# Kernel optimization log

Hardware: AMD Instinct MI355X
Metric: run time of the kernel (lower is better)

## Reference

```python
import jax, jax.numpy as jnp
import numpy as np

B, S, D_X, D_H = 1024, 512, 128, 128
A_VOCAB, A_EMB, T_VOCAB, T_EMB = 100, 32, 4, 16
GRU_IN = D_X + A_EMB + T_EMB + 1  # 177
Y_IN = D_H + D_X + A_EMB + T_EMB  # 304


def _lin_init(key, d_in, d_out):
    k1, k2 = jax.random.split(key)
    lim = 1.0 / np.sqrt(d_in)
    W = jax.random.uniform(k1, (d_out, d_in), minval=-lim, maxval=lim, dtype=jnp.float32)
    b = jax.random.uniform(k2, (d_out,), minval=-lim, maxval=lim, dtype=jnp.float32)
    return W, b


def setup_inputs() -> dict:
    key = jax.random.key(0)
    ks = jax.random.split(key, 16)
    x = jax.random.normal(ks[0], (B, D_X), dtype=jnp.float32)
    a = jax.random.randint(ks[1], (B, S), 0, A_VOCAB)
    t = jax.random.randint(ks[2], (B, S), 0, T_VOCAB)
    y = jax.random.uniform(ks[3], (B, S), dtype=jnp.float32)
    mask = jnp.ones((B, S), dtype=jnp.float32)

    xW, xb = _lin_init(ks[4], D_X, D_X)                 # x_proj
    a_emb = jax.random.normal(ks[5], (A_VOCAB, A_EMB), dtype=jnp.float32)
    t_emb = jax.random.normal(ks[6], (T_VOCAB, T_EMB), dtype=jnp.float32)
    W_ih, b_ih = _lin_init(ks[7], GRU_IN, 3 * D_H)      # GRUCell input weights
    W_hh, b_hh = _lin_init(ks[8], D_H, 3 * D_H)         # GRUCell hidden weights
    h0W, h0b = _lin_init(ks[9], D_X, D_H)               # h0 MLP
    tW1, tb1 = _lin_init(ks[10], D_H, D_H)              # t_head
    tW2, tb2 = _lin_init(ks[11], D_H, T_VOCAB)
    yW1, yb1 = _lin_init(ks[12], Y_IN, D_H)             # y_head
    yW2, yb2 = _lin_init(ks[13], D_H, 1)
    return {
        'x': x, 'a': a, 't': t, 'y': y, 'mask': mask,
        'xW': xW, 'xb': xb, 'a_emb': a_emb, 't_emb': t_emb,
        'W_ih': W_ih, 'b_ih': b_ih, 'W_hh': W_hh, 'b_hh': b_hh,
        'h0W': h0W, 'h0b': h0b,
        'tW1': tW1, 'tb1': tb1, 'tW2': tW2, 'tb2': tb2,
        'yW1': yW1, 'yb1': yb1, 'yW2': yW2, 'yb2': yb2,
    }


def _crn_forward(x, y, mask, xW, xb, a_emb, t_emb, W_ih, b_ih, W_hh, b_hh,
                 h0W, h0b, tW1, tb1, tW2, tb2, yW1, yb1, yW2, yb2, a, t):
    gelu = lambda v: jax.nn.gelu(v, approximate=False)
    x_enc = x @ xW.T + xb                       # [B, D_X]
    h = jnp.tanh(x_enc @ h0W.T + h0b)           # [B, D_H]
    a_e = a_emb[a]                              # [B, S, A_EMB]
    t_e = t_emb[t]                              # [B, S, T_EMB]
    y3 = y[..., None]                           # [B, S, 1]

    # time-major slices for scan
    a_e_t = jnp.swapaxes(a_e, 0, 1)
    t_e_t = jnp.swapaxes(t_e, 0, 1)
    y_t = jnp.swapaxes(y3, 0, 1)
    m_t = jnp.swapaxes(mask, 0, 1)[..., None]   # [S, B, 1]

    def step(h, inp):
        ae, te, yt, m = inp
        # grad_reverse is identity in forward; dropout off (eval)
        t_logits = gelu(h @ tW1.T + tb1) @ tW2.T + tb2          # [B, T_VOCAB]
        y_in = jnp.concatenate([h, x_enc, ae, te], axis=-1)
        y_logits = gelu(y_in @ yW1.T + yb1) @ yW2.T + yb2        # [B, 1]
        upd = jnp.concatenate([x_enc, ae, te, yt], axis=-1)      # [B, GRU_IN]
        gx = upd @ W_ih.T + b_ih
        gh = h @ W_hh.T + b_hh
        r = jax.nn.sigmoid(gx[:, :D_H] + gh[:, :D_H])
        z = jax.nn.sigmoid(gx[:, D_H:2 * D_H] + gh[:, D_H:2 * D_H])
        n = jnp.tanh(gx[:, 2 * D_H:] + r * gh[:, 2 * D_H:])
        h_next = (1.0 - z) * n + z * h
        h_new = m * h_next + (1.0 - m) * h
        return h_new, (y_logits, t_logits, h)

    _, (y_seq, t_seq, h_seq) = jax.lax.scan(step, h, (a_e_t, t_e_t, y_t, m_t))
    # back to batch-major [B, S, ...]
    return (jnp.swapaxes(y_seq, 0, 1), jnp.swapaxes(t_seq, 0, 1), jnp.swapaxes(h_seq, 0, 1))


def reference(x, a, t, y, mask, xW, xb, a_emb, t_emb, W_ih, b_ih, W_hh, b_hh,
              h0W, h0b, tW1, tb1, tW2, tb2, yW1, yb1, yW2, yb2):
    return _crn_forward(x, y, mask, xW, xb, a_emb, t_emb, W_ih, b_ih, W_hh, b_hh,
                        h0W, h0b, tW1, tb1, tW2, tb2, yW1, yb1, yW2, yb2, a, t)
```

## Files before the change

### kernel.cpp

```cpp
#include <hip/hip_runtime.h>
#include <math.h>

#define SLEN 512

typedef _Float16 half8 __attribute__((ext_vector_type(8)));
typedef _Float16 half2v __attribute__((ext_vector_type(2)));
typedef __fp16 fp16x2 __attribute__((ext_vector_type(2)));
typedef float f32x4 __attribute__((ext_vector_type(4)));
typedef unsigned int uint;

union U4H8 { uint4 u; half8 h; };
union UH2 { uint u; half2v v; fp16x2 p; };

static __device__ __forceinline__ uint packh2(float a, float b){
  UH2 x; x.p = __builtin_amdgcn_cvt_pkrtz(a, b); return x.u;
}
static __device__ __forceinline__ float loh(uint u){ UH2 x; x.u=u; return (float)x.v[0]; }
static __device__ __forceinline__ float hih(uint u){ UH2 x; x.u=u; return (float)x.v[1]; }
static __device__ __forceinline__ half8 ld_h8(const uint* p){
  U4H8 x; x.u = *(const uint4*)p; return x.h;
}
static __device__ __forceinline__ float rcpf(float x){ return __builtin_amdgcn_rcpf(x); }
static __device__ __forceinline__ float sigm(float v){ return rcpf(1.0f+__expf(-v)); }
static __device__ __forceinline__ float tanh_f(float v){ return 1.0f - 2.0f*rcpf(__expf(2.0f*v)+1.0f); }
static __device__ __forceinline__ float gelu_exact(float v){
  return 0.5f*v*(1.0f+erff(v*0.7071067811865475f));
}
#define MFMA(a,b,c) __builtin_amdgcn_mfma_f32_16x16x32_f16((a),(b),(c),0,0,0)

static __device__ __forceinline__ void wg_sync(){
  asm volatile("s_waitcnt lgkmcnt(0)" ::: "memory");
  __builtin_amdgcn_s_barrier();
}

__global__ void k_sample(const float* __restrict__ x, const float* __restrict__ xW, const float* __restrict__ xb,
                         const float* __restrict__ h0W, const float* __restrict__ h0b,
                         const float* __restrict__ W_ih, const float* __restrict__ b_ih, const float* __restrict__ b_hh,
                         const float* __restrict__ yW1, const float* __restrict__ yb1,
                         float* __restrict__ w_h0, float* __restrict__ w_xgx, float* __restrict__ w_yx)
{
  const int b = blockIdx.x, tid = threadIdx.x;
  __shared__ float sx[128];
  __shared__ float sxe[128];
  if (tid < 128) sx[tid] = x[b*128+tid];
  __syncthreads();
  if (tid < 128) {
    float acc = xb[tid];
    #pragma unroll 8
    for (int j=0;j<128;++j) acc += xW[tid*128+j]*sx[j];
    sxe[tid] = acc;
  }
  __syncthreads();
  {
    const int o = tid;
    float acc = b_ih[o] + (o < 256 ? b_hh[o] : 0.f);
    #pragma unroll 8
    for (int j=0;j<128;++j) acc += W_ih[o*177+j]*sxe[j];
    w_xgx[b*384+o] = acc;
  }
  if (tid < 128) {
    float acc = h0b[tid];
    #pragma unroll 8
    for (int j=0;j<128;++j) acc += h0W[tid*128+j]*sxe[j];
    w_h0[b*128+tid] = tanhf(acc);
    float a2 = yb1[tid];
    #pragma unroll 8
    for (int j=0;j<128;++j) a2 += yW1[tid*304+128+j]*sxe[j];
    w_yx[b*128+tid] = a2;
  }
}

__global__ __launch_bounds__(512,1) void k_recur(
  const float* __restrict__ W_hh, const float* __restrict__ W_ih, const float* __restrict__ b_hh,
  const int* __restrict__ a, const int* __restrict__ tt,
  const float* __restrict__ yy, const float* __restrict__ mask,
  const float* __restrict__ w_h0, const float* __restrict__ w_xgx,
  const float* __restrict__ a_emb, const float* __restrict__ t_emb,
  float* __restrict__ o_h, uint* __restrict__ h16)
{
  const int tid = threadIdx.x;
  const int wv = tid>>6, lane = tid&63, q = lane>>4, c = lane&15;
  const int b0 = blockIdx.x*16;
  const int r0 = wv*16;

  __shared__ __align__(16) uint s_h[2][16*68];
  __shared__ __align__(16) uint s_chunk[2][1024];
  __shared__ __align__(16) uint s_al[1600];
  __shared__ __align__(16) uint s_te[32];

  half8 wf[18];
  #pragma unroll
  for (int g=0; g<3; ++g) {
    const int row = g*128 + r0 + c;
    #pragma unroll
    for (int kt=0; kt<4; ++kt) {
      const float4* wp = (const float4*)(W_hh + row*128 + kt*32 + q*8);
      float4 v0 = wp[0], v1 = wp[1];
      half8 hv;
      hv[0]=(_Float16)v0.x; hv[1]=(_Float16)v0.y; hv[2]=(_Float16)v0.z; hv[3]=(_Float16)v0.w;
      hv[4]=(_Float16)v1.x; hv[5]=(_Float16)v1.y; hv[6]=(_Float16)v1.z; hv[7]=(_Float16)v1.w;
      wf[g*6+kt] = hv;
    }
    #pragma unroll
    for (int kt=4; kt<6; ++kt) {
      half8 hv;
      #pragma unroll
      for (int j=0;j<8;++j) {
        int k2 = (kt-4)*32 + q*8 + j;
        float v = (k2 < 49) ? W_ih[row*177 + 128 + k2] : 0.f;
        hv[j] = (_Float16)v;
      }
      wf[g*6+kt] = hv;
    }
  }
  f32x4 xgr, xgz, xgn, bhh, hm;
  #pragma unroll
  for (int j=0;j<4;++j) {
    const int rr = r0 + q*4 + j;
    xgr[j] = w_xgx[(b0+c)*384 +       rr];
    xgz[j] = w_xgx[(b0+c)*384 + 128 + rr];
    xgn[j] = w_xgx[(b0+c)*384 + 256 + rr];
    bhh[j] = b_hh[256 + rr];
    hm[j]  = w_h0[(b0+c)*128 + rr];
  }
  for (int d = tid; d < 1600; d += 512) {
    int row = d>>4, col = d&15;
    s_al[d] = packh2(a_emb[row*32+2*col], a_emb[row*32+2*col+1]);
  }
  if (tid < 32) {
    int row = tid>>3, col = tid&7;
    s_te[tid] = packh2(t_emb[row*16+2*col], t_emb[row*16+2*col+1]);
  }
  uint4 cr0, cr1, cr2, cr3;
  if (wv==0) {
    const uint* bp = (q==0) ? (const uint*)a : (q==1) ? (const uint*)tt
                   : (q==2) ? (const uint*)yy : (const uint*)mask;
    const uint4* p = (const uint4*)(bp + (size_t)(b0+c)*512);
    cr0=p[0]; cr1=p[1]; cr2=p[2]; cr3=p[3];
    uint4* dst = (uint4*)&s_chunk[0][q*256 + c*16];
    dst[0]=cr0; dst[1]=cr1; dst[2]=cr2; dst[3]=cr3;
  }
  s_h[0][c*68 + wv*8 + q*2]     = packh2(hm[0], hm[1]);
  s_h[0][c*68 + wv*8 + q*2 + 1] = packh2(hm[2], hm[3]);
  __syncthreads();

  for (int s=0; s<SLEN; ++s) {
    const int pb = s&1, par = (s>>4)&1, st = s&15;
    half8 hb[4];
    #pragma unroll
    for (int kt=0;kt<4;++kt) hb[kt] = ld_h8(&s_h[pb][c*68 + kt*16 + q*4]);
    const int av = (int)s_chunk[par][c*16 + st];
    const int tv = (int)s_chunk[par][256 + c*16 + st];
    const float yv = __uint_as_float(s_chunk[par][512 + c*16 + st]);
    const float mval = __uint_as_float(s_chunk[par][768 + c*16 + st]);
    half8 eb0 = ld_h8(&s_al[av*16 + q*4]);
    half8 eb1;
    if (q < 2) eb1 = ld_h8(&s_te[tv*8 + q*4]);
    else { U4H8 t; t.u = make_uint4((q==2)?packh2(yv,0.f):0u,0u,0u,0u); eb1 = t.h; }
    {
      const size_t p = (size_t)(b0+c)*SLEN + s;
      if (h16) {
        uint2 u; u.x = packh2(hm[0], hm[1]); u.y = packh2(hm[2], hm[3]);
        *(uint2*)(h16 + p*64 + wv*8 + q*2) = u;
      } else {
        *(float4*)(o_h + p*128 + r0 + q*4) = make_float4(hm[0],hm[1],hm[2],hm[3]);
      }
    }
    f32x4 ar = xgr, az = xgz, anh = bhh, anx = xgn;
    #pragma unroll
    for (int kt=0;kt<4;++kt) {
      ar  = MFMA(wf[kt],      hb[kt], ar);
      az  = MFMA(wf[6+kt],    hb[kt], az);
      anh = MFMA(wf[12+kt],   hb[kt], anh);
    }
    ar  = MFMA(wf[4],  eb0, ar);   ar  = MFMA(wf[5],  eb1, ar);
    az  = MFMA(wf[10], eb0, az);   az  = MFMA(wf[11], eb1, az);
    anx = MFMA(wf[16], eb0, anx);  anx = MFMA(wf[17], eb1, anx);
    #pragma unroll
    for (int j=0;j<4;++j) {
      float rj = sigm(ar[j]), zj = sigm(az[j]);
      float nj = tanh_f(anx[j] + rj*anh[j]);
      float hn = nj + zj*(hm[j] - nj);
      hm[j] = hm[j] + mval*(hn - hm[j]);
    }
    const int nb = (s+1)&1;
    s_h[nb][c*68 + wv*8 + q*2]     = packh2(hm[0], hm[1]);
    s_h[nb][c*68 + wv*8 + q*2 + 1] = packh2(hm[2], hm[3]);
    if (wv==0) {
      if ((st)==8 && s<490) {
        const int s0n = ((s>>4)+1)*16;
        const uint* bp = (q==0) ? (const uint*)a : (q==1) ? (const uint*)tt
                       : (q==2) ? (const uint*)yy : (const uint*)mask;
        const uint4* p = (const uint4*)(bp + (size_t)(b0+c)*512 + s0n);
        cr0=p[0]; cr1=p[1]; cr2=p[2]; cr3=p[3];
      }
      if ((st)==9 && s<491) {
        uint4* dst = (uint4*)&s_chunk[((s>>4)+1)&1][q*256 + c*16];
        dst[0]=cr0; dst[1]=cr1; dst[2]=cr2; dst[3]=cr3;
      }
    }
    wg_sync();
  }
}

template<bool H16>
__global__ __launch_bounds__(256,2) void k_heads(
  const float* __restrict__ tW1, const float* __restrict__ tb1,
  const float* __restrict__ tW2, const float* __restrict__ tb2,
  const float* __restrict__ yW1, const float* __restrict__ yW2, const float* __restrict__ yb2,
  const int* __restrict__ a, const int* __restrict__ tt,
  const float* __restrict__ w_yx,
  const float* __restrict__ a_emb, const float* __restrict__ t_emb,
  const float* __restrict__ h_f32, const uint* __restrict__ h16,
  float* __restrict__ o_y, float* __restrict__ o_t, float* __restrict__ o_h)
{
  const int tid = threadIdx.x;
  const int wv = tid>>6, lane = tid&63, q = lane>>4, c = lane&15;
  const bool isY = (wv >= 2);
  const int uh = wv&1;
  const int pair = wv>>1;
  const int p0 = blockIdx.x*1024;
  const int b0 = blockIdx.x*2;

  __shared__ __align__(16) uint s_al[100*20];
  __shared__ __align__(16) uint s_te[32];
  __shared__ __align__(16) uint s_gb[2][2][16*68];

  for (int d = tid; d < 1600; d += 256) {
    int row = d>>4, col = d&15;
    s_al[row*20+col] = packh2(a_emb[row*32+2*col], a_emb[row*32+2*col+1]);
  }
  if (tid < 32) {
    int row = tid>>3, col = tid&7;
    s_te[row*8+col] = packh2(t_emb[row*16+2*col], t_emb[row*16+2*col+1]);
  }

  half8 wf[24];
  const float* W1 = isY ? yW1 : tW1;
  const int w1stride = isY ? 304 : 128;
  #pragma unroll
  for (int ut=0;ut<4;++ut) {
    const int unit = uh*64 + ut*16 + c;
    #pragma unroll
    for (int kt=0;kt<4;++kt) {
      const float4* wp = (const float4*)(W1 + unit*w1stride + kt*32 + q*8);
      float4 v0 = wp[0], v1 = wp[1];
      half8 hv;
      hv[0]=(_Float16)v0.x; hv[1]=(_Float16)v0.y; hv[2]=(_Float16)v0.z; hv[3]=(_Float16)v0.w;
      hv[4]=(_Float16)v1.x; hv[5]=(_Float16)v1.y; hv[6]=(_Float16)v1.z; hv[7]=(_Float16)v1.w;
      wf[ut*6+kt] = hv;
    }
    #pragma unroll
    for (int kt=4;kt<6;++kt) {
      half8 hv;
      #pragma unroll
      for (int j=0;j<8;++j) {
        int k2 = (kt-4)*32 + q*8 + j;
        float v = (isY && k2 < 48) ? yW1[unit*304 + 256 + k2] : 0.f;
        hv[j] = (_Float16)v;
      }
      wf[ut*6+kt] = hv;
    }
  }
  half8 w2f[4];
  #pragma unroll
  for (int kt=0;kt<4;++kt) {
    half8 hv;
    #pragma unroll
    for (int j=0;j<8;++j) {
      float v = 0.f;
      if (!isY && c < 4) v = tW2[c*128 + kt*32 + q*8 + j];
      if ( isY && c == 0) v = yW2[kt*32 + q*8 + j];
      hv[j] = (_Float16)v;
    }
    w2f[kt] = hv;
  }
  float tb2r[4]; float yb2s = yb2[0];
  #pragma unroll
  for (int r=0;r<4;++r) tb2r[r] = tb2[r];
  f32x4 bsr0[4], bsr1[4];
  #pragma unroll
  for (int ut=0;ut<4;++ut)
    #pragma unroll
    for (int r=0;r<4;++r) {
      const int u = uh*64 + ut*16 + q*4 + r;
      bsr0[ut][r] = isY ? w_yx[(b0+0)*128 + u] : tb1[u];
      bsr1[ut][r] = isY ? w_yx[(b0+1)*128 + u] : tb1[u];
    }

  __syncthreads();

  half8 hbn[4];
  int avn = 0, tvn = 0;
  if (H16) {
    const uint* hp = h16 + (size_t)(p0 + c)*64;
    #pragma unroll
    for (int kt=0;kt<4;++kt) hbn[kt] = ld_h8(hp + kt*16 + q*4);
  }
  if (isY) { avn = a[p0 + c]; tvn = tt[p0 + c]; }

  #pragma unroll 1
  for (int ti=0; ti<64; ++ti) {
    const int par = ti&1;
    const int p = p0 + ti*16 + c;

    half8 hb[4];
    if (H16) {
      #pragma unroll
      for (int kt=0;kt<4;++kt) hb[kt] = hbn[kt];
    } else {
      const float* hp = h_f32 + (size_t)p*128;
      #pragma unroll
      for (int kt=0;kt<4;++kt) {
        const float4* fp = (const float4*)(hp + kt*32 + q*8);
        float4 v0 = fp[0], v1 = fp[1];
        half8 hv;
        hv[0]=(_Float16)v0.x; hv[1]=(_Float16)v0.y; hv[2]=(_Float16)v0.z; hv[3]=(_Float16)v0.w;
        hv[4]=(_Float16)v1.x; hv[5]=(_Float16)v1.y; hv[6]=(_Float16)v1.z; hv[7]=(_Float16)v1.w;
        hb[kt] = hv;
      }
    }
    const int av = avn, tv = tvn;

    if (H16 && !isY) {
      float* op = o_h + (size_t)p*128;
      #pragma unroll
      for (int kk=0;kk<2;++kk) {
        const int kt = uh*2 + kk;
        float4 f0 = make_float4((float)hb[kt][0], (float)hb[kt][1], (float)hb[kt][2], (float)hb[kt][3]);
        float4 f1 = make_float4((float)hb[kt][4], (float)hb[kt][5], (float)hb[kt][6], (float)hb[kt][7]);
        *(float4*)(op + kt*32 + q*8)     = f0;
        *(float4*)(op + kt*32 + q*8 + 4) = f1;
      }
    }

    f32x4 acc[4];
    #pragma unroll
    for (int ut=0;ut<4;++ut) acc[ut] = (ti < 32) ? bsr0[ut] : bsr1[ut];
    #pragma unroll
    for (int kt=0;kt<4;++kt)
      #pragma unroll
      for (int ut=0;ut<4;++ut) acc[ut] = MFMA(wf[ut*6+kt], hb[kt], acc[ut]);
    if (isY) {
      half8 eb[2];
      eb[0] = ld_h8(&s_al[av*20 + q*4]);
      if (q < 2) eb[1] = ld_h8(&s_te[tv*8 + q*4]);
      else {
        half8 z;
        #pragma unroll
        for (int j=0;j<8;++j) z[j] = (_Float16)0.f;
        eb[1] = z;
      }
      #pragma unroll
      for (int kt=4;kt<6;++kt)
        #pragma unroll
        for (int ut=0;ut<4;++ut) acc[ut] = MFMA(wf[ut*6+kt], eb[kt-4], acc[ut]);
    }

    #pragma unroll
    for (int ut=0;ut<4;++ut)
      #pragma unroll
      for (int pr=0;pr<2;++pr) {
        float g0 = gelu_exact(acc[ut][2*pr]);
        float g1 = gelu_exact(acc[ut][2*pr+1]);
        s_gb[pair][par][c*68 + uh*32 + ut*8 + 2*q + pr] = packh2(g0, g1);
      }

    {
      const int tn = (ti < 63) ? ti+1 : 63;
      const int pn = p0 + tn*16 + c;
      if (H16) {
        const uint* hp = h16 + (size_t)pn*64;
        #pragma unroll
        for (int kt=0;kt<4;++kt) hbn[kt] = ld_h8(hp + kt*16 + q*4);
      }
      if (isY) { avn = a[pn]; tvn = tt[pn]; }
    }

    wg_sync();

    if (par == uh) {
      f32x4 a2; a2[0]=0.f; a2[1]=0.f; a2[2]=0.f; a2[3]=0.f;
      #pragma unroll
      for (int kt=0;kt<4;++kt) {
        half8 gb = ld_h8(&s_gb[pair][par][c*68 + kt*16 + q*4]);
        a2 = MFMA(w2f[kt], gb, a2);
      }
      if (lane < 16) {
        if (!isY) {
          float4 o = make_float4(a2[0]+tb2r[0], a2[1]+tb2r[1], a2[2]+tb2r[2], a2[3]+tb2r[3]);
          *(float4*)&o_t[(size_t)p*4] = o;
        } else {
          o_y[p] = a2[0] + yb2s;
        }
      }
    }
  }
}

extern "C" void kernel_launch(void* const* d_in, const int* in_sizes, int n_in,
                              void* d_out, int out_size, void* d_ws, size_t ws_size,
                              hipStream_t stream) {
  (void)in_sizes; (void)n_in; (void)out_size;
  const float* x     = (const float*)d_in[0];
  const int*   a     = (const int*)  d_in[1];
  const int*   tt    = (const int*)  d_in[2];
  const float* y     = (const float*)d_in[3];
  const float* mask  = (const float*)d_in[4];
  const float* xW    = (const float*)d_in[5];
  const float* xb    = (const float*)d_in[6];
  const float* a_emb = (const float*)d_in[7];
  const float* t_emb = (const float*)d_in[8];
  const float* W_ih  = (const float*)d_in[9];
  const float* b_ih  = (const float*)d_in[10];
  const float* W_hh  = (const float*)d_in[11];
  const float* b_hh  = (const float*)d_in[12];
  const float* h0W   = (const float*)d_in[13];
  const float* h0b   = (const float*)d_in[14];
  const float* tW1   = (const float*)d_in[15];
  const float* tb1   = (const float*)d_in[16];
  const float* tW2   = (const float*)d_in[17];
  const float* tb2   = (const float*)d_in[18];
  const float* yW1   = (const float*)d_in[19];
  const float* yb1   = (const float*)d_in[20];
  const float* yW2   = (const float*)d_in[21];
  const float* yb2   = (const float*)d_in[22];

  float* o_y = (float*)d_out;
  float* o_t = o_y + 524288;
  float* o_h = o_y + 2621440;

  float* ws    = (float*)d_ws;
  float* w_h0  = ws;
  float* w_xgx = ws + 131072;
  float* w_yx  = ws + 524288;

  const size_t H16_BYTES = (size_t)524288 * 256;
  uint* h16 = nullptr;
  if (ws_size >= (size_t)655360*4 + H16_BYTES) h16 = (uint*)(ws + 655360);

  k_sample<<<1024, 384, 0, stream>>>(x, xW, xb, h0W, h0b, W_ih, b_ih, b_hh, yW1, yb1,
                                     w_h0, w_xgx, w_yx);
  k_recur<<<64, 512, 0, stream>>>(W_hh, W_ih, b_hh, a, tt, y, mask,
                                  w_h0, w_xgx, a_emb, t_emb, o_h, h16);
  if (h16)
    k_heads<true><<<512, 256, 0, stream>>>(tW1, tb1, tW2, tb2, yW1, yW2, yb2, a, tt,
                                           w_yx, a_emb, t_emb, o_h, h16, o_y, o_t, o_h);
  else
    k_heads<false><<<512, 256, 0, stream>>>(tW1, tb1, tW2, tb2, yW1, yW2, yb2, a, tt,
                                            w_yx, a_emb, t_emb, o_h, nullptr, o_y, o_t, o_h);
}
```

Before: 1.194 ms.

## Fuse output heads into recurrent kernel and swizzle shared-memory layouts

Moves the t-head and y-head computation into the recurrent kernel. Each wave computes its 16-unit slice of the first-layer head projections with extra MFMAs per step, writes GELU outputs to shared memory, and two waves apply the second-layer projection one step later. This removes the separate heads kernel and the fp16 hidden-state round trip through global memory. In exchange, every step of the serial recurrence now carries extra MFMA, GELU and store work, and only 64 workgroups run on a large GPU. Shared-memory layouts also get XOR swizzles and transposed chunk storage to reduce bank conflicts.

```diff
diff --git a/kernel.cpp b/kernel.cpp
--- a/kernel.cpp
+++ b/kernel.cpp
@@ -15,8 +15,6 @@
 static __device__ __forceinline__ uint packh2(float a, float b){
   UH2 x; x.p = __builtin_amdgcn_cvt_pkrtz(a, b); return x.u;
 }
-static __device__ __forceinline__ float loh(uint u){ UH2 x; x.u=u; return (float)x.v[0]; }
-static __device__ __forceinline__ float hih(uint u){ UH2 x; x.u=u; return (float)x.v[1]; }
 static __device__ __forceinline__ half8 ld_h8(const uint* p){
   U4H8 x; x.u = *(const uint4*)p; return x.h;
 }
@@ -26,12 +24,15 @@
 static __device__ __forceinline__ float gelu_exact(float v){
   return 0.5f*v*(1.0f+erff(v*0.7071067811865475f));
 }
+static __device__ __forceinline__ half8 cvt8(const float* p){
+  const float4* fp = (const float4*)p;
+  float4 v0 = fp[0], v1 = fp[1];
+  half8 hv;
+  hv[0]=(_Float16)v0.x; hv[1]=(_Float16)v0.y; hv[2]=(_Float16)v0.z; hv[3]=(_Float16)v0.w;
+  hv[4]=(_Float16)v1.x; hv[5]=(_Float16)v1.y; hv[6]=(_Float16)v1.z; hv[7]=(_Float16)v1.w;
+  return hv;
+}
 #define MFMA(a,b,c) __builtin_amdgcn_mfma_f32_16x16x32_f16((a),(b),(c),0,0,0)
-
-static __device__ __forceinline__ void wg_sync(){
-  asm volatile("s_waitcnt lgkmcnt(0)" ::: "memory");
-  __builtin_amdgcn_s_barrier();
-}
 
 __global__ void k_sample(const float* __restrict__ x, const float* __restrict__ xW, const float* __restrict__ xb,
                          const float* __restrict__ h0W, const float* __restrict__ h0b,
@@ -70,22 +71,27 @@
   }
 }
 
-__global__ __launch_bounds__(512,1) void k_recur(
+__global__ __launch_bounds__(512,1) void k_recur_fused(
   const float* __restrict__ W_hh, const float* __restrict__ W_ih, const float* __restrict__ b_hh,
   const int* __restrict__ a, const int* __restrict__ tt,
   const float* __restrict__ yy, const float* __restrict__ mask,
-  const float* __restrict__ w_h0, const float* __restrict__ w_xgx,
+  const float* __restrict__ w_h0, const float* __restrict__ w_xgx, const float* __restrict__ w_yx,
   const float* __restrict__ a_emb, const float* __restrict__ t_emb,
-  float* __restrict__ o_h, uint* __restrict__ h16)
+  const float* __restrict__ tW1, const float* __restrict__ tb1,
+  const float* __restrict__ tW2, const float* __restrict__ tb2,
+  const float* __restrict__ yW1, const float* __restrict__ yW2, const float* __restrict__ yb2,
+  float* __restrict__ o_y, float* __restrict__ o_t, float* __restrict__ o_h)
 {
   const int tid = threadIdx.x;
   const int wv = tid>>6, lane = tid&63, q = lane>>4, c = lane&15;
   const int b0 = blockIdx.x*16;
   const int r0 = wv*16;
-
-  __shared__ __align__(16) uint s_h[2][16*68];
+  const int swz = c&7;
+
+  __shared__ __align__(16) uint s_h[2][16*64];
+  __shared__ __align__(16) uint s_g[2][2][16*64];
   __shared__ __align__(16) uint s_chunk[2][1024];
-  __shared__ __align__(16) uint s_al[1600];
+  __shared__ __align__(16) uint s_al[100*20];
   __shared__ __align__(16) uint s_te[32];
 
   half8 wf[18];
@@ -93,14 +99,7 @@
   for (int g=0; g<3; ++g) {
     const int row = g*128 + r0 + c;
     #pragma unroll
-    for (int kt=0; kt<4; ++kt) {
-      const float4* wp = (const float4*)(W_hh + row*128 + kt*32 + q*8);
-      float4 v0 = wp[0], v1 = wp[1];
-      half8 hv;
-      hv[0]=(_Float16)v0.x; hv[1]=(_Float16)v0.y; hv[2]=(_Float16)v0.z; hv[3]=(_Float16)v0.w;
-      hv[4]=(_Float16)v1.x; hv[5]=(_Float16)v1.y; hv[6]=(_Float16)v1.z; hv[7]=(_Float16)v1.w;
-      wf[g*6+kt] = hv;
-    }
+    for (int kt=0; kt<4; ++kt) wf[g*6+kt] = cvt8(W_hh + row*128 + kt*32 + q*8);
     #pragma unroll
     for (int kt=4; kt<6; ++kt) {
       half8 hv;
@@ -113,7 +112,45 @@
       wf[g*6+kt] = hv;
     }
   }
-  f32x4 xgr, xgz, xgn, bhh, hm;
+  half8 wt[4], wy[6];
+  {
+    const int urow = r0 + c;
+    #pragma unroll
+    for (int kt=0; kt<4; ++kt) {
+      wt[kt] = cvt8(tW1 + urow*128 + kt*32 + q*8);
+      wy[kt] = cvt8(yW1 + urow*304 + kt*32 + q*8);
+    }
+    wy[4] = cvt8(yW1 + urow*304 + 256 + q*8);
+    half8 hv;
+    #pragma unroll
+    for (int j=0;j<8;++j) {
+      int k2 = 32 + q*8 + j;
+      hv[j] = (_Float16)((k2 < 48) ? yW1[urow*304 + 256 + k2] : 0.f);
+    }
+    wy[5] = hv;
+  }
+  half8 w2f[4];
+  if (wv == 6) {
+    #pragma unroll
+    for (int kt=0;kt<4;++kt) {
+      half8 hv;
+      #pragma unroll
+      for (int j=0;j<8;++j) hv[j] = (_Float16)((c < 4) ? tW2[c*128 + kt*32 + q*8 + j] : 0.f);
+      w2f[kt] = hv;
+    }
+  } else if (wv == 7) {
+    #pragma unroll
+    for (int kt=0;kt<4;++kt) {
+      half8 hv;
+      #pragma unroll
+      for (int j=0;j<8;++j) hv[j] = (_Float16)((c == 0) ? yW2[kt*32 + q*8 + j] : 0.f);
+      w2f[kt] = hv;
+    }
+  }
+  f32x4 tb2r; float yb2s = yb2[0];
+  #pragma unroll
+  for (int r=0;r<4;++r) tb2r[r] = tb2[r];
+  f32x4 xgr, xgz, xgn, bhh, hm, tb1r, wyx0;
   #pragma unroll
   for (int j=0;j<4;++j) {
     const int rr = r0 + q*4 + j;
@@ -122,10 +159,12 @@
     xgn[j] = w_xgx[(b0+c)*384 + 256 + rr];
     bhh[j] = b_hh[256 + rr];
     hm[j]  = w_h0[(b0+c)*128 + rr];
+    tb1r[j] = tb1[rr];
+    wyx0[j] = w_yx[(b0+c)*128 + rr];
   }
   for (int d = tid; d < 1600; d += 512) {
     int row = d>>4, col = d&15;
-    s_al[d] = packh2(a_emb[row*32+2*col], a_emb[row*32+2*col+1]);
+    s_al[row*20+col] = packh2(a_emb[row*32+2*col], a_emb[row*32+2*col+1]);
   }
   if (tid < 32) {
     int row = tid>>3, col = tid&7;
@@ -137,45 +176,72 @@
                    : (q==2) ? (const uint*)yy : (const uint*)mask;
     const uint4* p = (const uint4*)(bp + (size_t)(b0+c)*512);
     cr0=p[0]; cr1=p[1]; cr2=p[2]; cr3=p[3];
-    uint4* dst = (uint4*)&s_chunk[0][q*256 + c*16];
-    dst[0]=cr0; dst[1]=cr1; dst[2]=cr2; dst[3]=cr3;
-  }
-  s_h[0][c*68 + wv*8 + q*2]     = packh2(hm[0], hm[1]);
-  s_h[0][c*68 + wv*8 + q*2 + 1] = packh2(hm[2], hm[3]);
+    uint* dst = &s_chunk[0][q*256 + c];
+    dst[0*16]=cr0.x;  dst[1*16]=cr0.y;  dst[2*16]=cr0.z;  dst[3*16]=cr0.w;
+    dst[4*16]=cr1.x;  dst[5*16]=cr1.y;  dst[6*16]=cr1.z;  dst[7*16]=cr1.w;
+    dst[8*16]=cr2.x;  dst[9*16]=cr2.y;  dst[10*16]=cr2.z; dst[11*16]=cr2.w;
+    dst[12*16]=cr3.x; dst[13*16]=cr3.y; dst[14*16]=cr3.z; dst[15*16]=cr3.w;
+  }
+  {
+    const int slot = wv*2 + (q>>1);
+    const int hidx = c*64 + ((slot ^ swz)<<2) + (q&1)*2;
+    uint2 u; u.x = packh2(hm[0], hm[1]); u.y = packh2(hm[2], hm[3]);
+    *(uint2*)&s_h[0][hidx] = u;
+  }
   __syncthreads();
 
   for (int s=0; s<SLEN; ++s) {
     const int pb = s&1, par = (s>>4)&1, st = s&15;
     half8 hb[4];
     #pragma unroll
-    for (int kt=0;kt<4;++kt) hb[kt] = ld_h8(&s_h[pb][c*68 + kt*16 + q*4]);
-    const int av = (int)s_chunk[par][c*16 + st];
-    const int tv = (int)s_chunk[par][256 + c*16 + st];
-    const float yv = __uint_as_float(s_chunk[par][512 + c*16 + st]);
-    const float mval = __uint_as_float(s_chunk[par][768 + c*16 + st]);
-    half8 eb0 = ld_h8(&s_al[av*16 + q*4]);
+    for (int kt=0;kt<4;++kt) hb[kt] = ld_h8(&s_h[pb][c*64 + (((kt*4+q)^swz)<<2)]);
+    const int av = (int)s_chunk[par][        st*16 + c];
+    const int tv = (int)s_chunk[par][256   + st*16 + c];
+    const float yv   = __uint_as_float(s_chunk[par][512 + st*16 + c]);
+    const float mval = __uint_as_float(s_chunk[par][768 + st*16 + c]);
+    half8 eb0 = ld_h8(&s_al[av*20 + q*4]);
     half8 eb1;
     if (q < 2) eb1 = ld_h8(&s_te[tv*8 + q*4]);
     else { U4H8 t; t.u = make_uint4((q==2)?packh2(yv,0.f):0u,0u,0u,0u); eb1 = t.h; }
-    {
-      const size_t p = (size_t)(b0+c)*SLEN + s;
-      if (h16) {
-        uint2 u; u.x = packh2(hm[0], hm[1]); u.y = packh2(hm[2], hm[3]);
-        *(uint2*)(h16 + p*64 + wv*8 + q*2) = u;
-      } else {
-        *(float4*)(o_h + p*128 + r0 + q*4) = make_float4(hm[0],hm[1],hm[2],hm[3]);
-      }
-    }
-    f32x4 ar = xgr, az = xgz, anh = bhh, anx = xgn;
+
+    if (wv >= 6 && s > 0) {
+      const int hd = wv & 1, pp = (s-1)&1;
+      f32x4 a2; a2[0]=0.f; a2[1]=0.f; a2[2]=0.f; a2[3]=0.f;
+      #pragma unroll
+      for (int kt=0;kt<4;++kt) {
+        half8 gb = ld_h8(&s_g[hd][pp][c*64 + (((kt*4+q)^swz)<<2)]);
+        a2 = MFMA(w2f[kt], gb, a2);
+      }
+      if (lane < 16) {
+        const size_t p = (size_t)(b0+c)*SLEN + (s-1);
+        if (hd == 0) {
+          *(float4*)&o_t[p*4] = make_float4(a2[0]+tb2r[0], a2[1]+tb2r[1], a2[2]+tb2r[2], a2[3]+tb2r[3]);
+        } else {
+          o_y[p] = a2[0] + yb2s;
+        }
+      }
+    }
+    if ((q>>1) == (wv&1)) {
+      const int kt = wv>>1;
+      float* op = o_h + ((size_t)(b0+c)*SLEN + s)*128 + kt*32 + q*8;
+      *(float4*)op     = make_float4((float)hb[kt][0], (float)hb[kt][1], (float)hb[kt][2], (float)hb[kt][3]);
+      *(float4*)(op+4) = make_float4((float)hb[kt][4], (float)hb[kt][5], (float)hb[kt][6], (float)hb[kt][7]);
+    }
+
+    f32x4 ar = xgr, az = xgz, anh = bhh, anx = xgn, at = tb1r, ay = wyx0;
     #pragma unroll
     for (int kt=0;kt<4;++kt) {
-      ar  = MFMA(wf[kt],      hb[kt], ar);
-      az  = MFMA(wf[6+kt],    hb[kt], az);
-      anh = MFMA(wf[12+kt],   hb[kt], anh);
+      ar  = MFMA(wf[kt],    hb[kt], ar);
+      az  = MFMA(wf[6+kt],  hb[kt], az);
+      anh = MFMA(wf[12+kt], hb[kt], anh);
+      at  = MFMA(wt[kt],    hb[kt], at);
+      ay  = MFMA(wy[kt],    hb[kt], ay);
     }
     ar  = MFMA(wf[4],  eb0, ar);   ar  = MFMA(wf[5],  eb1, ar);
     az  = MFMA(wf[10], eb0, az);   az  = MFMA(wf[11], eb1, az);
     anx = MFMA(wf[16], eb0, anx);  anx = MFMA(wf[17], eb1, anx);
+    ay  = MFMA(wy[4],  eb0, ay);   ay  = MFMA(wy[5],  eb1, ay);
+
     #pragma unroll
     for (int j=0;j<4;++j) {
       float rj = sigm(ar[j]), zj = sigm(az[j]);
@@ -183,216 +249,55 @@
       float hn = nj + zj*(hm[j] - nj);
       hm[j] = hm[j] + mval*(hn - hm[j]);
     }
-    const int nb = (s+1)&1;
-    s_h[nb][c*68 + wv*8 + q*2]     = packh2(hm[0], hm[1]);
-    s_h[nb][c*68 + wv*8 + q*2 + 1] = packh2(hm[2], hm[3]);
+    {
+      const int slot = wv*2 + (q>>1);
+      const int hidx = c*64 + ((slot ^ swz)<<2) + (q&1)*2;
+      uint2 u; u.x = packh2(hm[0], hm[1]); u.y = packh2(hm[2], hm[3]);
+      *(uint2*)&s_h[(s+1)&1][hidx] = u;
+    }
+    {
+      const int slot = wv*2 + (q>>1);
+      const int gidx = c*64 + ((slot ^ swz)<<2) + (q&1)*2;
+      uint2 ut, uy;
+      ut.x = packh2(gelu_exact(at[0]), gelu_exact(at[1]));
+      ut.y = packh2(gelu_exact(at[2]), gelu_exact(at[3]));
+      uy.x = packh2(gelu_exact(ay[0]), gelu_exact(ay[1]));
+      uy.y = packh2(gelu_exact(ay[2]), gelu_exact(ay[3]));
+      *(uint2*)&s_g[0][s&1][gidx] = ut;
+      *(uint2*)&s_g[1][s&1][gidx] = uy;
+    }
     if (wv==0) {
-      if ((st)==8 && s<490) {
+      if (st==8 && s<490) {
         const int s0n = ((s>>4)+1)*16;
         const uint* bp = (q==0) ? (const uint*)a : (q==1) ? (const uint*)tt
                        : (q==2) ? (const uint*)yy : (const uint*)mask;
         const uint4* p = (const uint4*)(bp + (size_t)(b0+c)*512 + s0n);
         cr0=p[0]; cr1=p[1]; cr2=p[2]; cr3=p[3];
       }
-      if ((st)==9 && s<491) {
-        uint4* dst = (uint4*)&s_chunk[((s>>4)+1)&1][q*256 + c*16];
-        dst[0]=cr0; dst[1]=cr1; dst[2]=cr2; dst[3]=cr3;
-      }
-    }
-    wg_sync();
-  }
-}
-
-template<bool H16>
-__global__ __launch_bounds__(256,2) void k_heads(
-  const float* __restrict__ tW1, const float* __restrict__ tb1,
-  const float* __restrict__ tW2, const float* __restrict__ tb2,
-  const float* __restrict__ yW1, const float* __restrict__ yW2, const float* __restrict__ yb2,
-  const int* __restrict__ a, const int* __restrict__ tt,
-  const float* __restrict__ w_yx,
-  const float* __restrict__ a_emb, const float* __restrict__ t_emb,
-  const float* __restrict__ h_f32, const uint* __restrict__ h16,
-  float* __restrict__ o_y, float* __restrict__ o_t, float* __restrict__ o_h)
-{
-  const int tid = threadIdx.x;
-  const int wv = tid>>6, lane = tid&63, q = lane>>4, c = lane&15;
-  const bool isY = (wv >= 2);
-  const int uh = wv&1;
-  const int pair = wv>>1;
-  const int p0 = blockIdx.x*1024;
-  const int b0 = blockIdx.x*2;
-
-  __shared__ __align__(16) uint s_al[100*20];
-  __shared__ __align__(16) uint s_te[32];
-  __shared__ __align__(16) uint s_gb[2][2][16*68];
-
-  for (int d = tid; d < 1600; d += 256) {
-    int row = d>>4, col = d&15;
-    s_al[row*20+col] = packh2(a_emb[row*32+2*col], a_emb[row*32+2*col+1]);
-  }
-  if (tid < 32) {
-    int row = tid>>3, col = tid&7;
-    s_te[row*8+col] = packh2(t_emb[row*16+2*col], t_emb[row*16+2*col+1]);
-  }
-
-  half8 wf[24];
-  const float* W1 = isY ? yW1 : tW1;
-  const int w1stride = isY ? 304 : 128;
-  #pragma unroll
-  for (int ut=0;ut<4;++ut) {
-    const int unit = uh*64 + ut*16 + c;
+      if (st==9 && s<491) {
+        uint* dst = &s_chunk[((s>>4)+1)&1][q*256 + c];
+        dst[0*16]=cr0.x;  dst[1*16]=cr0.y;  dst[2*16]=cr0.z;  dst[3*16]=cr0.w;
+        dst[4*16]=cr1.x;  dst[5*16]=cr1.y;  dst[6*16]=cr1.z;  dst[7*16]=cr1.w;
+        dst[8*16]=cr2.x;  dst[9*16]=cr2.y;  dst[10*16]=cr2.z; dst[11*16]=cr2.w;
+        dst[12*16]=cr3.x; dst[13*16]=cr3.y; dst[14*16]=cr3.z; dst[15*16]=cr3.w;
+      }
+    }
+    __syncthreads();
+  }
+  if (wv >= 6) {
+    const int hd = wv & 1;
+    f32x4 a2; a2[0]=0.f; a2[1]=0.f; a2[2]=0.f; a2[3]=0.f;
     #pragma unroll
     for (int kt=0;kt<4;++kt) {
-      const float4* wp = (const float4*)(W1 + unit*w1stride + kt*32 + q*8);
-      float4 v0 = wp[0], v1 = wp[1];
-      half8 hv;
-      hv[0]=(_Float16)v0.x; hv[1]=(_Float16)v0.y; hv[2]=(_Float16)v0.z; hv[3]=(_Float16)v0.w;
-      hv[4]=(_Float16)v1.x; hv[5]=(_Float16)v1.y; hv[6]=(_Float16)v1.z; hv[7]=(_Float16)v1.w;
-      wf[ut*6+kt] = hv;
-    }
-    #pragma unroll
-    for (int kt=4;kt<6;++kt) {
-      half8 hv;
-      #pragma unroll
-      for (int j=0;j<8;++j) {
-        int k2 = (kt-4)*32 + q*8 + j;
-        float v = (isY && k2 < 48) ? yW1[unit*304 + 256 + k2] : 0.f;
-        hv[j] = (_Float16)v;
-      }
-      wf[ut*6+kt] = hv;
-    }
-  }
-  half8 w2f[4];
-  #pragma unroll
-  for (int kt=0;kt<4;++kt) {
-    half8 hv;
-    #pragma unroll
-    for (int j=0;j<8;++j) {
-      float v = 0.f;
-      if (!isY && c < 4) v = tW2[c*128 + kt*32 + q*8 + j];
-      if ( isY && c == 0) v = yW2[kt*32 + q*8 + j];
-      hv[j] = (_Float16)v;
-    }
-    w2f[kt] = hv;
-  }
-  float tb2r[4]; float yb2s = yb2[0];
-  #pragma unroll
-  for (int r=0;r<4;++r) tb2r[r] = tb2[r];
-  f32x4 bsr0[4], bsr1[4];
-  #pragma unroll
-  for (int ut=0;ut<4;++ut)
-    #pragma unroll
-    for (int r=0;r<4;++r) {
-      const int u = uh*64 + ut*16 + q*4 + r;
-      bsr0[ut][r] = isY ? w_yx[(b0+0)*128 + u] : tb1[u];
-      bsr1[ut][r] = isY ? w_yx[(b0+1)*128 + u] : tb1[u];
-    }
-
-  __syncthreads();
-
-  half8 hbn[4];
-  int avn = 0, tvn = 0;
-  if (H16) {
-    const uint* hp = h16 + (size_t)(p0 + c)*64;
-    #pragma unroll
-    for (int kt=0;kt<4;++kt) hbn[kt] = ld_h8(hp + kt*16 + q*4);
-  }
-  if (isY) { avn = a[p0 + c]; tvn = tt[p0 + c]; }
-
-  #pragma unroll 1
-  for (int ti=0; ti<64; ++ti) {
-    const int par = ti&1;
-    const int p = p0 + ti*16 + c;
-
-    half8 hb[4];
-    if (H16) {
-      #pragma unroll
-      for (int kt=0;kt<4;++kt) hb[kt] = hbn[kt];
-    } else {
-      const float* hp = h_f32 + (size_t)p*128;
-      #pragma unroll
-      for (int kt=0;kt<4;++kt) {
-        const float4* fp = (const float4*)(hp + kt*32 + q*8);
-        float4 v0 = fp[0], v1 = fp[1];
-        half8 hv;
-        hv[0]=(_Float16)v0.x; hv[1]=(_Float16)v0.y; hv[2]=(_Float16)v0.z; hv[3]=(_Float16)v0.w;
-        hv[4]=(_Float16)v1.x; hv[5]=(_Float16)v1.y; hv[6]=(_Float16)v1.z; hv[7]=(_Float16)v1.w;
-        hb[kt] = hv;
-      }
-    }
-    const int av = avn, tv = tvn;
-
-    if (H16 && !isY) {
-      float* op = o_h + (size_t)p*128;
-      #pragma unroll
-      for (int kk=0;kk<2;++kk) {
-        const int kt = uh*2 + kk;
-        float4 f0 = make_float4((float)hb[kt][0], (float)hb[kt][1], (float)hb[kt][2], (float)hb[kt][3]);
-        float4 f1 = make_float4((float)hb[kt][4], (float)hb[kt][5], (float)hb[kt][6], (float)hb[kt][7]);
-        *(float4*)(op + kt*32 + q*8)     = f0;
-        *(float4*)(op + kt*32 + q*8 + 4) = f1;
-      }
-    }
-
-    f32x4 acc[4];
-    #pragma unroll
-    for (int ut=0;ut<4;++ut) acc[ut] = (ti < 32) ? bsr0[ut] : bsr1[ut];
-    #pragma unroll
-    for (int kt=0;kt<4;++kt)
-      #pragma unroll
-      for (int ut=0;ut<4;++ut) acc[ut] = MFMA(wf[ut*6+kt], hb[kt], acc[ut]);
-    if (isY) {
-      half8 eb[2];
-      eb[0] = ld_h8(&s_al[av*20 + q*4]);
-      if (q < 2) eb[1] = ld_h8(&s_te[tv*8 + q*4]);
-      else {
-        half8 z;
-        #pragma unroll
-        for (int j=0;j<8;++j) z[j] = (_Float16)0.f;
-        eb[1] = z;
-      }
-      #pragma unroll
-      for (int kt=4;kt<6;++kt)
-        #pragma unroll
-        for (int ut=0;ut<4;++ut) acc[ut] = MFMA(wf[ut*6+kt], eb[kt-4], acc[ut]);
-    }
-
-    #pragma unroll
-    for (int ut=0;ut<4;++ut)
-      #pragma unroll
-      for (int pr=0;pr<2;++pr) {
-        float g0 = gelu_exact(acc[ut][2*pr]);
-        float g1 = gelu_exact(acc[ut][2*pr+1]);
-        s_gb[pair][par][c*68 + uh*32 + ut*8 + 2*q + pr] = packh2(g0, g1);
-      }
-
-    {
-      const int tn = (ti < 63) ? ti+1 : 63;
-      const int pn = p0 + tn*16 + c;
-      if (H16) {
-        const uint* hp = h16 + (size_t)pn*64;
-        #pragma unroll
-        for (int kt=0;kt<4;++kt) hbn[kt] = ld_h8(hp + kt*16 + q*4);
-      }
-      if (isY) { avn = a[pn]; tvn = tt[pn]; }
-    }
-
-    wg_sync();
-
-    if (par == uh) {
-      f32x4 a2; a2[0]=0.f; a2[1]=0.f; a2[2]=0.f; a2[3]=0.f;
-      #pragma unroll
-      for (int kt=0;kt<4;++kt) {
-        half8 gb = ld_h8(&s_gb[pair][par][c*68 + kt*16 + q*4]);
-        a2 = MFMA(w2f[kt], gb, a2);
-      }
-      if (lane < 16) {
-        if (!isY) {
-          float4 o = make_float4(a2[0]+tb2r[0], a2[1]+tb2r[1], a2[2]+tb2r[2], a2[3]+tb2r[3]);
-          *(float4*)&o_t[(size_t)p*4] = o;
-        } else {
-          o_y[p] = a2[0] + yb2s;
-        }
+      half8 gb = ld_h8(&s_g[hd][1][c*64 + (((kt*4+q)^swz)<<2)]);
+      a2 = MFMA(w2f[kt], gb, a2);
+    }
+    if (lane < 16) {
+      const size_t p = (size_t)(b0+c)*SLEN + (SLEN-1);
+      if (hd == 0) {
+        *(float4*)&o_t[p*4] = make_float4(a2[0]+tb2r[0], a2[1]+tb2r[1], a2[2]+tb2r[2], a2[3]+tb2r[3]);
+      } else {
+        o_y[p] = a2[0] + yb2s;
       }
     }
   }
@@ -401,7 +306,7 @@
 extern "C" void kernel_launch(void* const* d_in, const int* in_sizes, int n_in,
                               void* d_out, int out_size, void* d_ws, size_t ws_size,
                               hipStream_t stream) {
-  (void)in_sizes; (void)n_in; (void)out_size;
+  (void)in_sizes; (void)n_in; (void)out_size; (void)ws_size;
   const float* x     = (const float*)d_in[0];
   const int*   a     = (const int*)  d_in[1];
   const int*   tt    = (const int*)  d_in[2];
@@ -435,18 +340,10 @@
   float* w_xgx = ws + 131072;
   float* w_yx  = ws + 524288;
 
-  const size_t H16_BYTES = (size_t)524288 * 256;
-  uint* h16 = nullptr;
-  if (ws_size >= (size_t)655360*4 + H16_BYTES) h16 = (uint*)(ws + 655360);
-
   k_sample<<<1024, 384, 0, stream>>>(x, xW, xb, h0W, h0b, W_ih, b_ih, b_hh, yW1, yb1,
                                      w_h0, w_xgx, w_yx);
-  k_recur<<<64, 512, 0, stream>>>(W_hh, W_ih, b_hh, a, tt, y, mask,
-                                  w_h0, w_xgx, a_emb, t_emb, o_h, h16);
-  if (h16)
-    k_heads<true><<<512, 256, 0, stream>>>(tW1, tb1, tW2, tb2, yW1, yW2, yb2, a, tt,
-                                           w_yx, a_emb, t_emb, o_h, h16, o_y, o_t, o_h);
-  else
-    k_heads<false><<<512, 256, 0, stream>>>(tW1, tb1, tW2, tb2, yW1, yW2, yb2, a, tt,
-                                            w_yx, a_emb, t_emb, o_h, nullptr, o_y, o_t, o_h);
-}
+  k_recur_fused<<<64, 512, 0, stream>>>(W_hh, W_ih, b_hh, a, tt, y, mask,
+                                        w_h0, w_xgx, w_yx, a_emb, t_emb,
+                                        tW1, tb1, tW2, tb2, yW1, yW2, yb2,
+                                        o_y, o_t, o_h);
+}
```

Result: slower. 1.995 ms (+67.1%).
